# Kernel optimization log

Hardware: AMD Instinct MI355X
Metric: run time of the kernel (lower is better)

Reference implementation:

```python
import jax, jax.numpy as jnp
import numpy as np

B, D, C, P, H, I, E, TOPK = 65536, 1024, 256, 32, 128, 32, 16, 2
FUSION = D + P  # 1056

def ln(x, g, b, eps=1e-5):
    m = jnp.mean(x, axis=-1, keepdims=True)
    v = jnp.mean((x - m) ** 2, axis=-1, keepdims=True)
    return (x - m) * jax.lax.rsqrt(v + eps) * g + b

def setup_inputs() -> dict:
    key = jax.random.key(0)
    ks = jax.random.split(key, 8)
    def w(k, shape):
        return jax.random.normal(k, shape, dtype=jnp.float32) * 0.02
    return {
        "x": jax.random.normal(ks[0], (B, D), dtype=jnp.float32),
        "context": jax.random.normal(ks[1], (B, C), dtype=jnp.float32),
        "en_g": jnp.ones((D,), jnp.float32), "en_b": jnp.zeros((D,), jnp.float32),
        "cn_g": jnp.ones((C,), jnp.float32), "cn_b": jnp.zeros((C,), jnp.float32),
        "cp1_w": w(ks[2], (C, P)), "cp1_b": jnp.zeros((P,), jnp.float32),
        "cp2_w": w(ks[3], (P, P)), "cp2_b": jnp.zeros((P,), jnp.float32),
        "cpn_g": jnp.ones((P,), jnp.float32), "cpn_b": jnp.zeros((P,), jnp.float32),
        "fn_g": jnp.ones((FUSION,), jnp.float32), "fn_b": jnp.zeros((FUSION,), jnp.float32),
        "gp1_w": w(ks[4], (FUSION, H)), "gp1_b": jnp.zeros((H,), jnp.float32),
        "ln1_g": jnp.ones((H,), jnp.float32), "ln1_b": jnp.zeros((H,), jnp.float32),
        "gp2_w": w(ks[5], (H, I)), "gp2_b": jnp.zeros((I,), jnp.float32),
        "ln2_g": jnp.ones((I,), jnp.float32), "ln2_b": jnp.zeros((I,), jnp.float32),
        "gp3_w": w(ks[6], (I, E)), "gp3_b": jnp.zeros((E,), jnp.float32),
    }

def reference(x, context, en_g, en_b, cn_g, cn_b, cp1_w, cp1_b, cp2_w, cp2_b,
              cpn_g, cpn_b, fn_g, fn_b, gp1_w, gp1_b, ln1_g, ln1_b,
              gp2_w, gp2_b, ln2_g, ln2_b, gp3_w, gp3_b):
    gelu = lambda t: jax.nn.gelu(t, approximate=False)  # torch default GELU (erf)
    emb = ln(x, en_g, en_b)                               # [B, D]
    ctx = ln(context, cn_g, cn_b)                         # [B, C]
    cf = gelu(ctx @ cp1_w + cp1_b) @ cp2_w + cp2_b        # [B, P]
    cf = ln(cf, cpn_g, cpn_b)
    fusion = ln(jnp.concatenate([emb, cf], axis=-1), fn_g, fn_b)  # [B, FUSION]
    h = gelu(ln(fusion @ gp1_w + gp1_b, ln1_g, ln1_b))    # [B, H]
    inter = gelu(ln(h @ gp2_w + gp2_b, ln2_g, ln2_b))     # [B, I]
    clean_logits = inter @ gp3_w + gp3_b                  # [B, E]
    # inference path: no noise injection (training=False)
    top_v, top_i = jax.lax.top_k(clean_logits, TOPK)
    combined_weights = jax.nn.softmax(top_v / 1.0, axis=-1)  # temperature=1.0
    return combined_weights, top_i, clean_logits
```

## Files before the change

kernel.cpp:

```cpp
#include <hip/hip_runtime.h>
#include <math.h>

namespace {

using s8v = __attribute__((ext_vector_type(8))) short;
using vf4 = __attribute__((ext_vector_type(4))) float;

constexpr int Bn = 65536;
constexpr int Rn = 64;

constexpr size_t OFF_A1H  = 0;
constexpr size_t OFF_A1M  = 270336;
constexpr size_t OFF_A1L  = 540672;
constexpr size_t OFF_C1H  = 811008;
constexpr size_t OFF_C1M  = 827392;
constexpr size_t OFF_C1L  = 843776;
constexpr size_t OFF_C2H  = 860160;
constexpr size_t OFF_C2M  = 862208;
constexpr size_t OFF_C2L  = 864256;
constexpr size_t OFF_G2H  = 866304;
constexpr size_t OFF_G2M  = 874496;
constexpr size_t OFF_G2L  = 882688;
constexpr size_t OFF_VPK  = 890880;
constexpr size_t OFF_UPK  = 892928;
constexpr size_t OFF_CST  = 893184;
constexpr size_t OFF_VPART= 893216;

__device__ __forceinline__ unsigned short bf16_rn(float f) {
    unsigned u = __float_as_uint(f);
    u += 0x7FFFu + ((u >> 16) & 1u);
    return (unsigned short)(u >> 16);
}
__device__ __forceinline__ float bf16_tof(unsigned short h) {
    return __uint_as_float(((unsigned)h) << 16);
}

union S8U { s8v v; unsigned short u[8]; };

__device__ __forceinline__ vf4 MFMA(s8v a, s8v b, vf4 c) {
    return __builtin_amdgcn_mfma_f32_16x16x32_bf16(a, b, c, 0, 0, 0);
}

__device__ __forceinline__ void mfma6(vf4& acc, s8v ah, s8v am, s8v al,
                                      s8v bh, s8v bm, s8v bl) {
    acc = MFMA(ah, bh, acc);
    acc = MFMA(ah, bm, acc);
    acc = MFMA(am, bh, acc);
    acc = MFMA(ah, bl, acc);
    acc = MFMA(al, bh, acc);
    acc = MFMA(am, bm, acc);
}

__device__ __forceinline__ void split3(float v, unsigned short& h,
                                       unsigned short& m, unsigned short& l) {
    h = bf16_rn(v);
    const float r = v - bf16_tof(h);
    m = bf16_rn(r);
    const float r2 = r - bf16_tof(m);
    l = bf16_rn(r2);
}

__device__ __forceinline__ float gelu_f(float v) {
    return 0.5f * v * (1.0f + erff(v * 0.70710678118654752440f));
}

__device__ __forceinline__ void red16(float& s) {
    s += __shfl_xor(s, 1, 64); s += __shfl_xor(s, 2, 64);
    s += __shfl_xor(s, 4, 64); s += __shfl_xor(s, 8, 64);
}

__global__ void cag_prek1(const float* __restrict__ gp1_w,
                          const float* __restrict__ en_g, const float* __restrict__ en_b,
                          const float* __restrict__ fn_g, const float* __restrict__ fn_b,
                          char* __restrict__ ws)
{
    const int t = threadIdx.x, ch = blockIdx.x;
    s8v* A1h = (s8v*)(ws + OFF_A1H);
    s8v* A1m = (s8v*)(ws + OFF_A1M);
    s8v* A1l = (s8v*)(ws + OFF_A1L);
    float* Vpart = (float*)(ws + OFF_VPART);

    for (int s = t; s < 512; s += 256) {
        const int nt = s >> 6, lane = s & 63;
        const int n = nt * 16 + (lane & 15);
        const int jb = ch * 32 + 8 * (lane >> 4);
        S8U h, m, lo;
        #pragma unroll
        for (int r = 0; r < 8; ++r) {
            const int j = jb + r;
            const float sc = fn_g[j] * (j < 1024 ? en_g[j] : 1.0f);
            const float a = sc * gp1_w[(size_t)j * 128 + n];
            split3(a, h.u[r], m.u[r], lo.u[r]);
        }
        A1h[(ch * 8 + nt) * 64 + lane] = h.v;
        A1m[(ch * 8 + nt) * 64 + lane] = m.v;
        A1l[(ch * 8 + nt) * 64 + lane] = lo.v;
    }
    if (t < 128) {
        float v1 = 0.f, v2 = 0.f, v3 = 0.f, v4 = 0.f;
        for (int jj = 0; jj < 32; ++jj) {
            const int j = ch * 32 + jj;
            const float wv = gp1_w[(size_t)j * 128 + t];
            const float fg = fn_g[j];
            if (j < 1024) { v1 = fmaf(fg * en_g[j], wv, v1); v2 = fmaf(fg * en_b[j], wv, v2); }
            v3 = fmaf(fg, wv, v3);
            v4 = fmaf(fn_b[j], wv, v4);
        }
        float* p = Vpart + ((size_t)ch * 128 + t) * 4;
        p[0] = v1; p[1] = v2; p[2] = v3; p[3] = v4;
    }
}

__global__ void cag_prek2(const float* __restrict__ en_g, const float* __restrict__ en_b,
                          const float* __restrict__ cn_g, const float* __restrict__ cn_b,
                          const float* __restrict__ cp1_w, const float* __restrict__ cp1_b,
                          const float* __restrict__ cp2_w, const float* __restrict__ gp2_w,
                          const float* __restrict__ gp1_b,
                          char* __restrict__ ws)
{
    const int t = threadIdx.x, b = blockIdx.x;
    if (b == 0) {
        const float* Vpart = (const float*)(ws + OFF_VPART);
        float* Vpk = (float*)(ws + OFF_VPK);
        float* cst = (float*)(ws + OFF_CST);
        if (t < 128) {
            float v1 = 0.f, v2 = 0.f, v3 = 0.f, v4 = 0.f;
            for (int ch = 0; ch < 33; ++ch) {
                const float* p = Vpart + ((size_t)ch * 128 + t) * 4;
                v1 += p[0]; v2 += p[1]; v3 += p[2]; v4 += p[3];
            }
            v4 += gp1_b[t];
            float* q = Vpk + t * 4;
            q[0] = v1; q[1] = v2; q[2] = v3; q[3] = v4;
        }
        __shared__ float red[256];
        float part[5] = {0.f, 0.f, 0.f, 0.f, 0.f};
        for (int i = t; i < 1024; i += 256) {
            const float g = en_g[i], bb = en_b[i];
            part[0] += g; part[1] += bb; part[2] += g * g; part[3] += g * bb; part[4] += bb * bb;
        }
        for (int f = 0; f < 5; ++f) {
            red[t] = part[f]; __syncthreads();
            for (int s = 128; s > 0; s >>= 1) { if (t < s) red[t] += red[t + s]; __syncthreads(); }
            if (t == 0) cst[f] = red[0];
            __syncthreads();
        }
    } else if (b == 1) {
        s8v* C1h = (s8v*)(ws + OFF_C1H);
        s8v* C1m = (s8v*)(ws + OFF_C1M);
        s8v* C1l = (s8v*)(ws + OFF_C1L);
        float* up = (float*)(ws + OFF_UPK);
        for (int s = t; s < 8 * 2 * 64; s += 256) {
            const int ks = s >> 7, nt = (s >> 6) & 1, lane = s & 63;
            const int n = nt * 16 + (lane & 15);
            const int kb = ks * 32 + 8 * (lane >> 4);
            S8U h, m, lo;
            #pragma unroll
            for (int r = 0; r < 8; ++r) {
                const int k = kb + r;
                const float a = cn_g[k] * cp1_w[k * 32 + n];
                split3(a, h.u[r], m.u[r], lo.u[r]);
            }
            C1h[(ks * 2 + nt) * 64 + lane] = h.v;
            C1m[(ks * 2 + nt) * 64 + lane] = m.v;
            C1l[(ks * 2 + nt) * 64 + lane] = lo.v;
        }
        if (t < 32) {
            float u1 = 0.f, u2 = 0.f;
            for (int c = 0; c < 256; ++c) {
                u1 = fmaf(cn_g[c], cp1_w[c * 32 + t], u1);
                u2 = fmaf(cn_b[c], cp1_w[c * 32 + t], u2);
            }
            up[2 * t] = u1; up[2 * t + 1] = u2 + cp1_b[t];
        }
    } else if (b == 2) {
        s8v* C2h = (s8v*)(ws + OFF_C2H);
        s8v* C2m = (s8v*)(ws + OFF_C2M);
        s8v* C2l = (s8v*)(ws + OFF_C2L);
        if (t < 128) {
            const int nt = t >> 6, lane = t & 63;
            const int n = nt * 16 + (lane & 15);
            const int kb = 8 * (lane >> 4);
            S8U h, m, lo;
            #pragma unroll
            for (int r = 0; r < 8; ++r) {
                const float a = cp2_w[(kb + r) * 32 + n];
                split3(a, h.u[r], m.u[r], lo.u[r]);
            }
            C2h[nt * 64 + lane] = h.v;
            C2m[nt * 64 + lane] = m.v;
            C2l[nt * 64 + lane] = lo.v;
        }
    } else {
        s8v* G2h = (s8v*)(ws + OFF_G2H);
        s8v* G2m = (s8v*)(ws + OFF_G2M);
        s8v* G2l = (s8v*)(ws + OFF_G2L);
        for (int s = t; s < 4 * 2 * 64; s += 256) {
            const int ks = s >> 7, nt = (s >> 6) & 1, lane = s & 63;
            const int n = nt * 16 + (lane & 15);
            const int kb = ks * 32 + 8 * (lane >> 4);
            S8U h, m, lo;
            #pragma unroll
            for (int r = 0; r < 8; ++r) {
                const float a = gp2_w[(kb + r) * 32 + n];
                split3(a, h.u[r], m.u[r], lo.u[r]);
            }
            G2h[(ks * 2 + nt) * 64 + lane] = h.v;
            G2m[(ks * 2 + nt) * 64 + lane] = m.v;
            G2l[(ks * 2 + nt) * 64 + lane] = lo.v;
        }
    }
}

__global__ __launch_bounds__(256, 2)
void cag_main(const float* __restrict__ x, const float* __restrict__ ctx,
              const float* __restrict__ en_g, const float* __restrict__ en_b,
              const float* __restrict__ cpn_g, const float* __restrict__ cpn_b,
              const float* __restrict__ cp2_b,
              const float* __restrict__ ln1_g, const float* __restrict__ ln1_b,
              const float* __restrict__ gp2_b,
              const float* __restrict__ ln2_g, const float* __restrict__ ln2_b,
              const float* __restrict__ gp3_w, const float* __restrict__ gp3_b,
              const char* __restrict__ ws, float* __restrict__ out)
{
    __shared__ __attribute__((aligned(16))) char smU[64 * 132 * 4];
    __shared__ float cfnbuf[64][36];
    __shared__ float s_sc4[64][4];
    __shared__ float part_s[4][64];
    __shared__ float part_s2[4][64];
    __shared__ float s_ln1[64][2];
    __shared__ float s_cfs[64], s_cfs2[64];

    short (*fragA)[3][4][64][8] = (short(*)[3][4][64][8])smU;
    float (*pbuf)[36]  = (float(*)[36])smU;
    float (*hbuf)[132] = (float(*)[132])smU;
    float (*ibuf)[36]  = (float(*)[36])smU;
    float (*lbuf)[20]  = (float(*)[20])(smU + 16384);

    const int tid = threadIdx.x;
    const int l = tid & 63, w = tid >> 6;
    const int sg = l >> 4, lr = l & 15;
    const int row0 = blockIdx.x * Rn;

    const s8v* A1h = (const s8v*)(ws + OFF_A1H);
    const s8v* A1m = (const s8v*)(ws + OFF_A1M);
    const s8v* A1l = (const s8v*)(ws + OFF_A1L);
    const s8v* C1h = (const s8v*)(ws + OFF_C1H);
    const s8v* C1m = (const s8v*)(ws + OFF_C1M);
    const s8v* C1l = (const s8v*)(ws + OFF_C1L);
    const s8v* C2h = (const s8v*)(ws + OFF_C2H);
    const s8v* C2m = (const s8v*)(ws + OFF_C2M);
    const s8v* C2l = (const s8v*)(ws + OFF_C2L);
    const s8v* G2h = (const s8v*)(ws + OFF_G2H);
    const s8v* G2m = (const s8v*)(ws + OFF_G2M);
    const s8v* G2l = (const s8v*)(ws + OFF_G2L);
    const float* Vpk = (const float*)(ws + OFF_VPK);
    const float* upk = (const float*)(ws + OFF_UPK);
    const float* cst = (const float*)(ws + OFF_CST);

    {
        const int crow = row0 + 16 * w + lr;
        const float* cb = ctx + (size_t)crow * 256 + 8 * sg;
        float cs = 0.f, cs2 = 0.f;
        vf4 ac0 = {0.f, 0.f, 0.f, 0.f}, ac1 = {0.f, 0.f, 0.f, 0.f};
        #pragma unroll
        for (int ks = 0; ks < 8; ++ks) {
            const float4 a0 = *(const float4*)(cb + ks * 32);
            const float4 a1 = *(const float4*)(cb + ks * 32 + 4);
            const float vv[8] = {a0.x, a0.y, a0.z, a0.w, a1.x, a1.y, a1.z, a1.w};
            S8U ah, am, al;
            #pragma unroll
            for (int j = 0; j < 8; ++j) {
                const float v = vv[j];
                cs += v; cs2 = fmaf(v, v, cs2);
                split3(v, ah.u[j], am.u[j], al.u[j]);
            }
            mfma6(ac0, ah.v, am.v, al.v,
                  C1h[(ks * 2 + 0) * 64 + l], C1m[(ks * 2 + 0) * 64 + l], C1l[(ks * 2 + 0) * 64 + l]);
            mfma6(ac1, ah.v, am.v, al.v,
                  C1h[(ks * 2 + 1) * 64 + l], C1m[(ks * 2 + 1) * 64 + l], C1l[(ks * 2 + 1) * 64 + l]);
        }
        cs += __shfl_xor(cs, 16, 64); cs += __shfl_xor(cs, 32, 64);
        cs2 += __shfl_xor(cs2, 16, 64); cs2 += __shfl_xor(cs2, 32, 64);
        const float cm = cs * (1.f / 256.f);
        const float crr = rsqrtf(cs2 * (1.f / 256.f) - cm * cm + 1e-5f);
        float m_r[4], r_r[4];
        #pragma unroll
        for (int rg = 0; rg < 4; ++rg) {
            const int src = 4 * sg + rg;
            m_r[rg] = __shfl(cm, src, 64);
            r_r[rg] = __shfl(crr, src, 64);
        }
        #pragma unroll
        for (int ntl = 0; ntl < 2; ++ntl) {
            const int c = 16 * ntl + lr;
            const float u1 = upk[2 * c], u2 = upk[2 * c + 1];
            #pragma unroll
            for (int rg = 0; rg < 4; ++rg) {
                const float av = (ntl == 0) ? ac0[rg] : ac1[rg];
                const float a1v = r_r[rg] * av - r_r[rg] * m_r[rg] * u1 + u2;
                pbuf[16 * w + 4 * sg + rg][c] = gelu_f(a1v);
            }
        }
        __syncthreads();
        float pv[8];
        const int prow = 16 * w + lr;
        *(float4*)&pv[0] = *(const float4*)&pbuf[prow][8 * sg];
        *(float4*)&pv[4] = *(const float4*)&pbuf[prow][8 * sg + 4];
        S8U ph, pm_, pl;
        #pragma unroll
        for (int j = 0; j < 8; ++j) split3(pv[j], ph.u[j], pm_.u[j], pl.u[j]);
        vf4 a20 = {0.f, 0.f, 0.f, 0.f}, a21 = {0.f, 0.f, 0.f, 0.f};
        mfma6(a20, ph.v, pm_.v, pl.v, C2h[0 * 64 + l], C2m[0 * 64 + l], C2l[0 * 64 + l]);
        mfma6(a21, ph.v, pm_.v, pl.v, C2h[1 * 64 + l], C2m[1 * 64 + l], C2l[1 * 64 + l]);
        const float cb0 = cp2_b[lr], cb1 = cp2_b[16 + lr];
        const float cg0 = cpn_g[lr], cg1 = cpn_g[16 + lr];
        const float cbb0 = cpn_b[lr], cbb1 = cpn_b[16 + lr];
        #pragma unroll
        for (int rg = 0; rg < 4; ++rg) {
            const float v0 = a20[rg] + cb0, v1 = a21[rg] + cb1;
            float s = v0 + v1, s2 = v0 * v0 + v1 * v1;
            red16(s); red16(s2);
            const float pm = s * (1.f / 32.f);
            const float prs = rsqrtf(s2 * (1.f / 32.f) - pm * pm + 1e-5f);
            const float cn0 = (v0 - pm) * prs * cg0 + cbb0;
            const float cn1 = (v1 - pm) * prs * cg1 + cbb1;
            float t = cn0 + cn1, t2 = cn0 * cn0 + cn1 * cn1;
            red16(t); red16(t2);
            const int rr = 16 * w + 4 * sg + rg;
            if (lr == 0) { s_cfs[rr] = t; s_cfs2[rr] = t2; }
            cfnbuf[rr][lr] = cn0; cfnbuf[rr][16 + lr] = cn1;
        }
    }
    __syncthreads();

    float Sx = 0.f, Sxx = 0.f, Sxg = 0.f, Sxg2 = 0.f, Sxgb = 0.f, Sxxg2 = 0.f;
    vf4 acc[4][2];
    #pragma unroll
    for (int mt = 0; mt < 4; ++mt) { acc[mt][0] = vf4{0.f,0.f,0.f,0.f}; acc[mt][1] = vf4{0.f,0.f,0.f,0.f}; }

    const float* xb = x + (size_t)(row0 + 16 * w + lr) * 1024 + 8 * sg;
    float xrinv = 0.f;

    auto stage_x = [&](int c, const float4& a0, const float4& a1) {
        const float vv[8] = {a0.x, a0.y, a0.z, a0.w, a1.x, a1.y, a1.z, a1.w};
        const float4 g0 = *(const float4*)(en_g + c * 32 + 8 * sg);
        const float4 g1 = *(const float4*)(en_g + c * 32 + 8 * sg + 4);
        const float4 e0 = *(const float4*)(en_b + c * 32 + 8 * sg);
        const float4 e1 = *(const float4*)(en_b + c * 32 + 8 * sg + 4);
        const float gg[8] = {g0.x, g0.y, g0.z, g0.w, g1.x, g1.y, g1.z, g1.w};
        const float eb[8] = {e0.x, e0.y, e0.z, e0.w, e1.x, e1.y, e1.z, e1.w};
        S8U hh, mm, ll;
        #pragma unroll
        for (int j = 0; j < 8; ++j) {
            const float v = vv[j], g = gg[j], b = eb[j];
            Sx += v; Sxx = fmaf(v, v, Sxx);
            const float tt = v * g;
            Sxg += tt; Sxg2 = fmaf(tt, g, Sxg2); Sxgb = fmaf(tt, b, Sxgb); Sxxg2 = fmaf(tt, tt, Sxxg2);
            split3(v, hh.u[j], mm.u[j], ll.u[j]);
        }
        *(s8v*)&fragA[c & 1][0][w][l][0] = hh.v;
        *(s8v*)&fragA[c & 1][1][w][l][0] = mm.v;
        *(s8v*)&fragA[c & 1][2][w][l][0] = ll.v;
    };

    {
        const float4 t0 = *(const float4*)(xb + 0), t1 = *(const float4*)(xb + 4);
        float4 xA0 = *(const float4*)(xb + 32), xA1 = *(const float4*)(xb + 36);
        stage_x(0, t0, t1);
        __syncthreads();

        const int nt0 = 2 * w, nt1 = 2 * w + 1;
        s8v bn0h = A1h[(0 * 8 + nt0) * 64 + l], bn0m = A1m[(0 * 8 + nt0) * 64 + l], bn0l = A1l[(0 * 8 + nt0) * 64 + l];
        s8v bn1h = A1h[(0 * 8 + nt1) * 64 + l], bn1m = A1m[(0 * 8 + nt1) * 64 + l], bn1l = A1l[(0 * 8 + nt1) * 64 + l];
        float4 xB0, xB1;

        #pragma unroll 1
        for (int ks = 0; ks <= 32; ++ks) {
            const s8v b0h = bn0h, b0m = bn0m, b0l = bn0l;
            const s8v b1h = bn1h, b1m = bn1m, b1l = bn1l;
            if (ks < 32) {
                bn0h = A1h[((ks + 1) * 8 + nt0) * 64 + l]; bn0m = A1m[((ks + 1) * 8 + nt0) * 64 + l]; bn0l = A1l[((ks + 1) * 8 + nt0) * 64 + l];
                bn1h = A1h[((ks + 1) * 8 + nt1) * 64 + l]; bn1m = A1m[((ks + 1) * 8 + nt1) * 64 + l]; bn1l = A1l[((ks + 1) * 8 + nt1) * 64 + l];
            }
            if (ks + 2 <= 31) {
                xB0 = *(const float4*)(xb + (ks + 2) * 32);
                xB1 = *(const float4*)(xb + (ks + 2) * 32 + 4);
            }
            #pragma unroll
            for (int mt = 0; mt < 4; ++mt) {
                const s8v ah = *(const s8v*)&fragA[ks & 1][0][mt][l][0];
                const s8v am = *(const s8v*)&fragA[ks & 1][1][mt][l][0];
                const s8v al = *(const s8v*)&fragA[ks & 1][2][mt][l][0];
                mfma6(acc[mt][0], ah, am, al, b0h, b0m, b0l);
                mfma6(acc[mt][1], ah, am, al, b1h, b1m, b1l);
            }
            if (ks == 31) {
                float sx = Sx, sxx = Sxx, sxg = Sxg, sxg2 = Sxg2, sxgb = Sxgb, sxxg2 = Sxxg2;
                sx += __shfl_xor(sx, 16, 64); sx += __shfl_xor(sx, 32, 64);
                sxx += __shfl_xor(sxx, 16, 64); sxx += __shfl_xor(sxx, 32, 64);
                sxg += __shfl_xor(sxg, 16, 64); sxg += __shfl_xor(sxg, 32, 64);
                sxg2 += __shfl_xor(sxg2, 16, 64); sxg2 += __shfl_xor(sxg2, 32, 64);
                sxgb += __shfl_xor(sxgb, 16, 64); sxgb += __shfl_xor(sxgb, 32, 64);
                sxxg2 += __shfl_xor(sxxg2, 16, 64); sxxg2 += __shfl_xor(sxxg2, 32, 64);
                const float xm = sx * (1.f / 1024.f);
                const float xvar = sxx * (1.f / 1024.f) - xm * xm;
                const float xr = rsqrtf(xvar + 1e-5f);
                xrinv = sqrtf(xvar + 1e-5f);
                const float Gs = cst[0], Bs = cst[1], Sg2c = cst[2], Sgbc = cst[3], Sb2c = cst[4];
                const float Semb = xr * (sxg - xm * Gs) + Bs;
                const float Semb2 = xr * xr * (sxxg2 - 2.f * xm * sxg2 + xm * xm * Sg2c)
                                  + 2.f * xr * (sxgb - xm * Sgbc) + Sb2c;
                const int rr = 16 * w + lr;
                const float fm = (Semb + s_cfs[rr]) * (1.f / 1056.f);
                const float fvar = (Semb2 + s_cfs2[rr]) * (1.f / 1056.f) - fm * fm;
                const float fr = rsqrtf(fvar + 1e-5f);
                if (sg == 0) {
                    s_sc4[rr][0] = fr * xr;
                    s_sc4[rr][1] = -fr * xr * xm;
                    s_sc4[rr][2] = fr;
                    s_sc4[rr][3] = -fr * fm;
                }
            }
            if (ks < 31) {
                stage_x(ks + 1, xA0, xA1);
                xA0 = xB0; xA1 = xB1;
            } else if (ks == 31) {
                const int rr = 16 * w + lr;
                float vv[8];
                *(float4*)&vv[0] = *(const float4*)&cfnbuf[rr][8 * sg];
                *(float4*)&vv[4] = *(const float4*)&cfnbuf[rr][8 * sg + 4];
                S8U hh, mm, ll;
                #pragma unroll
                for (int j = 0; j < 8; ++j) split3(vv[j] * xrinv, hh.u[j], mm.u[j], ll.u[j]);
                *(s8v*)&fragA[0][0][w][l][0] = hh.v;
                *(s8v*)&fragA[0][1][w][l][0] = mm.v;
                *(s8v*)&fragA[0][2][w][l][0] = ll.v;
            }
            __syncthreads();
        }
    }

    {
        float4 Vc[2];
        #pragma unroll
        for (int ntl = 0; ntl < 2; ++ntl)
            Vc[ntl] = *(const float4*)&Vpk[(16 * (2 * w + ntl) + lr) * 4];
        #pragma unroll
        for (int mt = 0; mt < 4; ++mt) {
            #pragma unroll
            for (int rg = 0; rg < 4; ++rg) {
                const float4 sc = *(const float4*)&s_sc4[16 * mt + 4 * sg + rg][0];
                #pragma unroll
                for (int ntl = 0; ntl < 2; ++ntl) {
                    acc[mt][ntl][rg] = sc.x * acc[mt][ntl][rg] + sc.y * Vc[ntl].x
                                     + sc.z * Vc[ntl].y + sc.w * Vc[ntl].z + Vc[ntl].w;
                }
            }
        }
        #pragma unroll
        for (int mt = 0; mt < 4; ++mt) {
            #pragma unroll
            for (int rg = 0; rg < 4; ++rg) {
                const float v0 = acc[mt][0][rg], v1 = acc[mt][1][rg];
                float s = v0 + v1, s2 = v0 * v0 + v1 * v1;
                red16(s); red16(s2);
                if (lr == 0) {
                    const int rr = 16 * mt + 4 * sg + rg;
                    part_s[w][rr] = s; part_s2[w][rr] = s2;
                }
            }
        }
        __syncthreads();
        if (tid < 64) {
            const float s = part_s[0][tid] + part_s[1][tid] + part_s[2][tid] + part_s[3][tid];
            const float s2 = part_s2[0][tid] + part_s2[1][tid] + part_s2[2][tid] + part_s2[3][tid];
            const float mn = s * (1.f / 128.f);
            s_ln1[tid][0] = mn;
            s_ln1[tid][1] = rsqrtf(s2 * (1.f / 128.f) - mn * mn + 1e-5f);
        }
        __syncthreads();
        float g1c[2], b1c[2];
        #pragma unroll
        for (int ntl = 0; ntl < 2; ++ntl) {
            const int c = 16 * (2 * w + ntl) + lr;
            g1c[ntl] = ln1_g[c]; b1c[ntl] = ln1_b[c];
        }
        #pragma unroll
        for (int mt = 0; mt < 4; ++mt) {
            #pragma unroll
            for (int rg = 0; rg < 4; ++rg) {
                const int rr = 16 * mt + 4 * sg + rg;
                const float mn = s_ln1[rr][0], rs = s_ln1[rr][1];
                #pragma unroll
                for (int ntl = 0; ntl < 2; ++ntl) {
                    const float hp = gelu_f((acc[mt][ntl][rg] - mn) * rs * g1c[ntl] + b1c[ntl]);
                    hbuf[rr][16 * (2 * w + ntl) + lr] = hp;
                }
            }
        }
        __syncthreads();
    }

    float iv[2][4];
    {
        vf4 aG0 = {0.f, 0.f, 0.f, 0.f}, aG1 = {0.f, 0.f, 0.f, 0.f};
        const int hrow = 16 * w + lr;
        #pragma unroll
        for (int ks = 0; ks < 4; ++ks) {
            float pv[8];
            *(float4*)&pv[0] = *(const float4*)&hbuf[hrow][ks * 32 + 8 * sg];
            *(float4*)&pv[4] = *(const float4*)&hbuf[hrow][ks * 32 + 8 * sg + 4];
            S8U ah, am, al;
            #pragma unroll
            for (int j = 0; j < 8; ++j) split3(pv[j], ah.u[j], am.u[j], al.u[j]);
            mfma6(aG0, ah.v, am.v, al.v,
                  G2h[(ks * 2 + 0) * 64 + l], G2m[(ks * 2 + 0) * 64 + l], G2l[(ks * 2 + 0) * 64 + l]);
            mfma6(aG1, ah.v, am.v, al.v,
                  G2h[(ks * 2 + 1) * 64 + l], G2m[(ks * 2 + 1) * 64 + l], G2l[(ks * 2 + 1) * 64 + l]);
        }
        const float gb0 = gp2_b[lr], gb1 = gp2_b[16 + lr];
        const float lg0 = ln2_g[lr], lg1 = ln2_g[16 + lr];
        const float lb0 = ln2_b[lr], lb1 = ln2_b[16 + lr];
        #pragma unroll
        for (int rg = 0; rg < 4; ++rg) {
            const float v0 = aG0[rg] + gb0, v1 = aG1[rg] + gb1;
            float s = v0 + v1, s2 = v0 * v0 + v1 * v1;
            red16(s); red16(s2);
            const float mn = s * (1.f / 32.f);
            const float rs = rsqrtf(s2 * (1.f / 32.f) - mn * mn + 1e-5f);
            iv[0][rg] = gelu_f((v0 - mn) * rs * lg0 + lb0);
            iv[1][rg] = gelu_f((v1 - mn) * rs * lg1 + lb1);
        }
    }
    __syncthreads();
    #pragma unroll
    for (int rg = 0; rg < 4; ++rg) {
        const int rr = 16 * w + 4 * sg + rg;
        ibuf[rr][lr] = iv[0][rg];
        ibuf[rr][16 + lr] = iv[1][rg];
    }
    __syncthreads();

    {
        const int r = tid >> 2, e4 = (tid & 3) * 4;
        float a0 = 0.f, a1 = 0.f, a2 = 0.f, a3 = 0.f;
        #pragma unroll 4
        for (int q = 0; q < 32; ++q) {
            const float v = ibuf[r][q];
            const float4 w3 = *(const float4*)(gp3_w + q * 16 + e4);
            a0 = fmaf(v, w3.x, a0); a1 = fmaf(v, w3.y, a1);
            a2 = fmaf(v, w3.z, a2); a3 = fmaf(v, w3.w, a3);
        }
        const float4 b3 = *(const float4*)(gp3_b + e4);
        const float4 lg = make_float4(a0 + b3.x, a1 + b3.y, a2 + b3.z, a3 + b3.w);
        float* outl = out + (size_t)Bn * 4;
        *(float4*)(outl + (size_t)(row0 + r) * 16 + e4) = lg;
        *(float4*)&lbuf[r][e4] = lg;
    }
    __syncthreads();
    if (tid < 64) {
        float v[16];
        #pragma unroll
        for (int e = 0; e < 4; ++e) *(float4*)&v[e * 4] = *(const float4*)&lbuf[tid][e * 4];
        int i0 = 0; float v0 = v[0];
        #pragma unroll
        for (int e = 1; e < 16; ++e) if (v[e] > v0) { v0 = v[e]; i0 = e; }
        int i1 = -1; float v1 = -3.4e38f;
        #pragma unroll
        for (int e = 0; e < 16; ++e) if (e != i0 && v[e] > v1) { v1 = v[e]; i1 = e; }
        const float e1 = expf(v1 - v0);
        const float inv = 1.0f / (1.0f + e1);
        const size_t g = (size_t)(row0 + tid);
        out[g * 2 + 0] = inv;
        out[g * 2 + 1] = e1 * inv;
        float* outi = out + (size_t)Bn * 2;
        outi[g * 2 + 0] = (float)i0;
        outi[g * 2 + 1] = (float)i1;
    }
}

}

extern "C" void kernel_launch(void* const* d_in, const int* in_sizes, int n_in,
                              void* d_out, int out_size, void* d_ws, size_t ws_size,
                              hipStream_t stream) {
    const float* x     = (const float*)d_in[0];
    const float* ctx   = (const float*)d_in[1];
    const float* en_g  = (const float*)d_in[2];
    const float* en_b  = (const float*)d_in[3];
    const float* cn_g  = (const float*)d_in[4];
    const float* cn_b  = (const float*)d_in[5];
    const float* cp1_w = (const float*)d_in[6];
    const float* cp1_b = (const float*)d_in[7];
    const float* cp2_w = (const float*)d_in[8];
    const float* cp2_b = (const float*)d_in[9];
    const float* cpn_g = (const float*)d_in[10];
    const float* cpn_b = (const float*)d_in[11];
    const float* fn_g  = (const float*)d_in[12];
    const float* fn_b  = (const float*)d_in[13];
    const float* gp1_w = (const float*)d_in[14];
    const float* gp1_b = (const float*)d_in[15];
    const float* ln1_g = (const float*)d_in[16];
    const float* ln1_b = (const float*)d_in[17];
    const float* gp2_w = (const float*)d_in[18];
    const float* gp2_b = (const float*)d_in[19];
    const float* ln2_g = (const float*)d_in[20];
    const float* ln2_b = (const float*)d_in[21];
    const float* gp3_w = (const float*)d_in[22];
    const float* gp3_b = (const float*)d_in[23];

    char* ws = (char*)d_ws;
    hipLaunchKernelGGL(cag_prek1, dim3(33), dim3(256), 0, stream,
                       gp1_w, en_g, en_b, fn_g, fn_b, ws);
    hipLaunchKernelGGL(cag_prek2, dim3(4), dim3(256), 0, stream,
                       en_g, en_b, cn_g, cn_b, cp1_w, cp1_b, cp2_w, gp2_w, gp1_b, ws);
    hipLaunchKernelGGL(cag_main, dim3(Bn / Rn), dim3(256), 0, stream,
                       x, ctx, en_g, en_b, cpn_g, cpn_b, cp2_b,
                       ln1_g, ln1_b, gp2_b, ln2_g, ln2_b, gp3_w, gp3_b,
                       ws, (float*)d_out);
}
```

Before: 212.2 us.

## Use 2x2 warp tiling for first GEMM with register-resident A fragments

Restructures the fusion GEMM so each warp computes a 32-row by 64-column tile: it loads and splits its own x rows directly into registers instead of staging them through shared memory. This removes the per-k-step __syncthreads and LDS round-trip for A, and halves the cross-warp LayerNorm partial reductions. In exchange each warp splits twice as many x values into bf16 pieces, repeating that work across column-warps, and holds more B fragments and accumulators in registers, raising register pressure at two blocks per CU.

Measured after the change: 230.3 us. 1.09x slower.

```diff
diff --git a/kernel.cpp b/kernel.cpp
--- a/kernel.cpp
+++ b/kernel.cpp
@@ -67,6 +67,24 @@
 __device__ __forceinline__ void red16(float& s) {
     s += __shfl_xor(s, 1, 64); s += __shfl_xor(s, 2, 64);
     s += __shfl_xor(s, 4, 64); s += __shfl_xor(s, 8, 64);
+}
+
+__device__ __forceinline__ void stageA(const float4& va, const float4& vb,
+    const float* gg, const float* ee,
+    float& Sx, float& Sxx, float& Sxg, float& Sxg2, float& Sxgb, float& Sq,
+    s8v& fh, s8v& fm, s8v& fl)
+{
+    const float vv[8] = {va.x, va.y, va.z, va.w, vb.x, vb.y, vb.z, vb.w};
+    S8U H, M, L;
+    #pragma unroll
+    for (int j = 0; j < 8; ++j) {
+        const float v = vv[j], g = gg[j], b = ee[j];
+        Sx += v; Sxx = fmaf(v, v, Sxx);
+        const float t = v * g;
+        Sxg += t; Sxg2 = fmaf(t, g, Sxg2); Sxgb = fmaf(t, b, Sxgb); Sq = fmaf(t, t, Sq);
+        split3(v, H.u[j], M.u[j], L.u[j]);
+    }
+    fh = H.v; fm = M.v; fl = L.v;
 }
 
 __global__ void cag_prek1(const float* __restrict__ gp1_w,
@@ -224,18 +242,16 @@
               const char* __restrict__ ws, float* __restrict__ out)
 {
     __shared__ __attribute__((aligned(16))) char smU[64 * 132 * 4];
-    __shared__ float cfnbuf[64][36];
     __shared__ float s_sc4[64][4];
-    __shared__ float part_s[4][64];
-    __shared__ float part_s2[4][64];
-    __shared__ float s_ln1[64][2];
+    __shared__ float part_s[2][64];
+    __shared__ float part_s2[2][64];
     __shared__ float s_cfs[64], s_cfs2[64];
 
-    short (*fragA)[3][4][64][8] = (short(*)[3][4][64][8])smU;
-    float (*pbuf)[36]  = (float(*)[36])smU;
-    float (*hbuf)[132] = (float(*)[132])smU;
-    float (*ibuf)[36]  = (float(*)[36])smU;
-    float (*lbuf)[20]  = (float(*)[20])(smU + 16384);
+    float (*pbuf)[36]   = (float(*)[36])smU;
+    float (*cfnbuf)[36] = (float(*)[36])(smU + 20480);
+    float (*hbuf)[132]  = (float(*)[132])smU;
+    float (*ibuf)[36]   = (float(*)[36])smU;
+    float (*lbuf)[20]   = (float(*)[20])(smU + 16384);
 
     const int tid = threadIdx.x;
     const int l = tid & 63, w = tid >> 6;
@@ -334,168 +350,190 @@
     }
     __syncthreads();
 
-    float Sx = 0.f, Sxx = 0.f, Sxg = 0.f, Sxg2 = 0.f, Sxgb = 0.f, Sxxg2 = 0.f;
-    vf4 acc[4][2];
+    const int a_ = w & 1, c_ = w >> 1;
+    const float* xb0 = x + (size_t)(row0 + 32 * a_ + lr) * 1024 + 8 * sg;
+    const float* xb1 = xb0 + 16 * 1024;
+
+    vf4 acc[2][4];
     #pragma unroll
-    for (int mt = 0; mt < 4; ++mt) { acc[mt][0] = vf4{0.f,0.f,0.f,0.f}; acc[mt][1] = vf4{0.f,0.f,0.f,0.f}; }
-
-    const float* xb = x + (size_t)(row0 + 16 * w + lr) * 1024 + 8 * sg;
-    float xrinv = 0.f;
-
-    auto stage_x = [&](int c, const float4& a0, const float4& a1) {
-        const float vv[8] = {a0.x, a0.y, a0.z, a0.w, a1.x, a1.y, a1.z, a1.w};
-        const float4 g0 = *(const float4*)(en_g + c * 32 + 8 * sg);
-        const float4 g1 = *(const float4*)(en_g + c * 32 + 8 * sg + 4);
-        const float4 e0 = *(const float4*)(en_b + c * 32 + 8 * sg);
-        const float4 e1 = *(const float4*)(en_b + c * 32 + 8 * sg + 4);
+    for (int mt = 0; mt < 2; ++mt)
+        #pragma unroll
+        for (int j = 0; j < 4; ++j) acc[mt][j] = vf4{0.f, 0.f, 0.f, 0.f};
+
+    float s0x = 0.f, s0xx = 0.f, s0xg = 0.f, s0xg2 = 0.f, s0xgb = 0.f, s0q = 0.f;
+    float s1x = 0.f, s1xx = 0.f, s1xg = 0.f, s1xg2 = 0.f, s1xgb = 0.f, s1q = 0.f;
+
+    s8v B0h, B0m, B0l, B1h, B1m, B1l, B2h, B2m, B2l, B3h, B3m, B3l;
+    {
+        const size_t q0 = (size_t)((4 * c_) * 64 + l);
+        B0h = A1h[q0]; B0m = A1m[q0]; B0l = A1l[q0];
+        B1h = A1h[q0 + 64]; B1m = A1m[q0 + 64]; B1l = A1l[q0 + 64];
+    }
+    float4 c0a = *(const float4*)(xb0);
+    float4 c0b = *(const float4*)(xb0 + 4);
+    float4 c1a = *(const float4*)(xb1);
+    float4 c1b = *(const float4*)(xb1 + 4);
+
+    s8v a0h, a0m, a0l, a1h, a1m, a1l;
+
+    #pragma unroll 1
+    for (int ks = 0; ks < 32; ++ks) {
+        const size_t o2 = (size_t)((ks * 8 + 4 * c_ + 2) * 64 + l);
+        B2h = A1h[o2]; B2m = A1m[o2]; B2l = A1l[o2];
+        B3h = A1h[o2 + 64]; B3m = A1m[o2 + 64]; B3l = A1l[o2 + 64];
+        const int kb = ks * 32 + 8 * sg;
+        const float4 g0 = *(const float4*)(en_g + kb);
+        const float4 g1 = *(const float4*)(en_g + kb + 4);
+        const float4 e0 = *(const float4*)(en_b + kb);
+        const float4 e1 = *(const float4*)(en_b + kb + 4);
+        float4 n0a, n0b, n1a, n1b;
+        if (ks < 31) {
+            n0a = *(const float4*)(xb0 + (ks + 1) * 32);
+            n0b = *(const float4*)(xb0 + (ks + 1) * 32 + 4);
+            n1a = *(const float4*)(xb1 + (ks + 1) * 32);
+            n1b = *(const float4*)(xb1 + (ks + 1) * 32 + 4);
+        }
         const float gg[8] = {g0.x, g0.y, g0.z, g0.w, g1.x, g1.y, g1.z, g1.w};
-        const float eb[8] = {e0.x, e0.y, e0.z, e0.w, e1.x, e1.y, e1.z, e1.w};
-        S8U hh, mm, ll;
-        #pragma unroll
-        for (int j = 0; j < 8; ++j) {
-            const float v = vv[j], g = gg[j], b = eb[j];
-            Sx += v; Sxx = fmaf(v, v, Sxx);
-            const float tt = v * g;
-            Sxg += tt; Sxg2 = fmaf(tt, g, Sxg2); Sxgb = fmaf(tt, b, Sxgb); Sxxg2 = fmaf(tt, tt, Sxxg2);
-            split3(v, hh.u[j], mm.u[j], ll.u[j]);
-        }
-        *(s8v*)&fragA[c & 1][0][w][l][0] = hh.v;
-        *(s8v*)&fragA[c & 1][1][w][l][0] = mm.v;
-        *(s8v*)&fragA[c & 1][2][w][l][0] = ll.v;
-    };
-
-    {
-        const float4 t0 = *(const float4*)(xb + 0), t1 = *(const float4*)(xb + 4);
-        float4 xA0 = *(const float4*)(xb + 32), xA1 = *(const float4*)(xb + 36);
-        stage_x(0, t0, t1);
-        __syncthreads();
-
-        const int nt0 = 2 * w, nt1 = 2 * w + 1;
-        s8v bn0h = A1h[(0 * 8 + nt0) * 64 + l], bn0m = A1m[(0 * 8 + nt0) * 64 + l], bn0l = A1l[(0 * 8 + nt0) * 64 + l];
-        s8v bn1h = A1h[(0 * 8 + nt1) * 64 + l], bn1m = A1m[(0 * 8 + nt1) * 64 + l], bn1l = A1l[(0 * 8 + nt1) * 64 + l];
-        float4 xB0, xB1;
-
-        #pragma unroll 1
-        for (int ks = 0; ks <= 32; ++ks) {
-            const s8v b0h = bn0h, b0m = bn0m, b0l = bn0l;
-            const s8v b1h = bn1h, b1m = bn1m, b1l = bn1l;
-            if (ks < 32) {
-                bn0h = A1h[((ks + 1) * 8 + nt0) * 64 + l]; bn0m = A1m[((ks + 1) * 8 + nt0) * 64 + l]; bn0l = A1l[((ks + 1) * 8 + nt0) * 64 + l];
-                bn1h = A1h[((ks + 1) * 8 + nt1) * 64 + l]; bn1m = A1m[((ks + 1) * 8 + nt1) * 64 + l]; bn1l = A1l[((ks + 1) * 8 + nt1) * 64 + l];
-            }
-            if (ks + 2 <= 31) {
-                xB0 = *(const float4*)(xb + (ks + 2) * 32);
-                xB1 = *(const float4*)(xb + (ks + 2) * 32 + 4);
-            }
-            #pragma unroll
-            for (int mt = 0; mt < 4; ++mt) {
-                const s8v ah = *(const s8v*)&fragA[ks & 1][0][mt][l][0];
-                const s8v am = *(const s8v*)&fragA[ks & 1][1][mt][l][0];
-                const s8v al = *(const s8v*)&fragA[ks & 1][2][mt][l][0];
-                mfma6(acc[mt][0], ah, am, al, b0h, b0m, b0l);
-                mfma6(acc[mt][1], ah, am, al, b1h, b1m, b1l);
-            }
-            if (ks == 31) {
-                float sx = Sx, sxx = Sxx, sxg = Sxg, sxg2 = Sxg2, sxgb = Sxgb, sxxg2 = Sxxg2;
-                sx += __shfl_xor(sx, 16, 64); sx += __shfl_xor(sx, 32, 64);
-                sxx += __shfl_xor(sxx, 16, 64); sxx += __shfl_xor(sxx, 32, 64);
-                sxg += __shfl_xor(sxg, 16, 64); sxg += __shfl_xor(sxg, 32, 64);
-                sxg2 += __shfl_xor(sxg2, 16, 64); sxg2 += __shfl_xor(sxg2, 32, 64);
-                sxgb += __shfl_xor(sxgb, 16, 64); sxgb += __shfl_xor(sxgb, 32, 64);
-                sxxg2 += __shfl_xor(sxxg2, 16, 64); sxxg2 += __shfl_xor(sxxg2, 32, 64);
-                const float xm = sx * (1.f / 1024.f);
-                const float xvar = sxx * (1.f / 1024.f) - xm * xm;
-                const float xr = rsqrtf(xvar + 1e-5f);
-                xrinv = sqrtf(xvar + 1e-5f);
-                const float Gs = cst[0], Bs = cst[1], Sg2c = cst[2], Sgbc = cst[3], Sb2c = cst[4];
-                const float Semb = xr * (sxg - xm * Gs) + Bs;
-                const float Semb2 = xr * xr * (sxxg2 - 2.f * xm * sxg2 + xm * xm * Sg2c)
-                                  + 2.f * xr * (sxgb - xm * Sgbc) + Sb2c;
-                const int rr = 16 * w + lr;
-                const float fm = (Semb + s_cfs[rr]) * (1.f / 1056.f);
-                const float fvar = (Semb2 + s_cfs2[rr]) * (1.f / 1056.f) - fm * fm;
-                const float fr = rsqrtf(fvar + 1e-5f);
-                if (sg == 0) {
-                    s_sc4[rr][0] = fr * xr;
-                    s_sc4[rr][1] = -fr * xr * xm;
-                    s_sc4[rr][2] = fr;
-                    s_sc4[rr][3] = -fr * fm;
+        const float ee[8] = {e0.x, e0.y, e0.z, e0.w, e1.x, e1.y, e1.z, e1.w};
+        stageA(c0a, c0b, gg, ee, s0x, s0xx, s0xg, s0xg2, s0xgb, s0q, a0h, a0m, a0l);
+        stageA(c1a, c1b, gg, ee, s1x, s1xx, s1xg, s1xg2, s1xgb, s1q, a1h, a1m, a1l);
+        mfma6(acc[0][0], a0h, a0m, a0l, B0h, B0m, B0l);
+        mfma6(acc[1][0], a1h, a1m, a1l, B0h, B0m, B0l);
+        mfma6(acc[0][1], a0h, a0m, a0l, B1h, B1m, B1l);
+        mfma6(acc[1][1], a1h, a1m, a1l, B1h, B1m, B1l);
+        const size_t p0 = (size_t)(((ks + 1) * 8 + 4 * c_) * 64 + l);
+        B0h = A1h[p0]; B0m = A1m[p0]; B0l = A1l[p0];
+        B1h = A1h[p0 + 64]; B1m = A1m[p0 + 64]; B1l = A1l[p0 + 64];
+        mfma6(acc[0][2], a0h, a0m, a0l, B2h, B2m, B2l);
+        mfma6(acc[1][2], a1h, a1m, a1l, B2h, B2m, B2l);
+        mfma6(acc[0][3], a0h, a0m, a0l, B3h, B3m, B3l);
+        mfma6(acc[1][3], a1h, a1m, a1l, B3h, B3m, B3l);
+        if (ks < 31) { c0a = n0a; c0b = n0b; c1a = n1a; c1b = n1b; }
+    }
+
+    {
+        #define RED2(s) { s += __shfl_xor(s, 16, 64); s += __shfl_xor(s, 32, 64); }
+        RED2(s0x) RED2(s0xx) RED2(s0xg) RED2(s0xg2) RED2(s0xgb) RED2(s0q)
+        RED2(s1x) RED2(s1xx) RED2(s1xg) RED2(s1xg2) RED2(s1xgb) RED2(s1q)
+        #undef RED2
+    }
+    const float Gs = cst[0], Bs = cst[1], Sg2c = cst[2], Sgbc = cst[3], Sb2c = cst[4];
+    float xrinv0, xrinv1;
+    {
+        const float xm = s0x * (1.f / 1024.f);
+        const float xv = s0xx * (1.f / 1024.f) - xm * xm;
+        const float xr = rsqrtf(xv + 1e-5f);
+        xrinv0 = sqrtf(xv + 1e-5f);
+        const float Semb = xr * (s0xg - xm * Gs) + Bs;
+        const float Semb2 = xr * xr * (s0q - 2.f * xm * s0xg2 + xm * xm * Sg2c)
+                          + 2.f * xr * (s0xgb - xm * Sgbc) + Sb2c;
+        const int rr = 32 * a_ + lr;
+        const float fm = (Semb + s_cfs[rr]) * (1.f / 1056.f);
+        const float fvar = (Semb2 + s_cfs2[rr]) * (1.f / 1056.f) - fm * fm;
+        const float fr = rsqrtf(fvar + 1e-5f);
+        if (sg == 0) {
+            s_sc4[rr][0] = fr * xr; s_sc4[rr][1] = -fr * xr * xm;
+            s_sc4[rr][2] = fr;      s_sc4[rr][3] = -fr * fm;
+        }
+    }
+    {
+        const float xm = s1x * (1.f / 1024.f);
+        const float xv = s1xx * (1.f / 1024.f) - xm * xm;
+        const float xr = rsqrtf(xv + 1e-5f);
+        xrinv1 = sqrtf(xv + 1e-5f);
+        const float Semb = xr * (s1xg - xm * Gs) + Bs;
+        const float Semb2 = xr * xr * (s1q - 2.f * xm * s1xg2 + xm * xm * Sg2c)
+                          + 2.f * xr * (s1xgb - xm * Sgbc) + Sb2c;
+        const int rr = 32 * a_ + 16 + lr;
+        const float fm = (Semb + s_cfs[rr]) * (1.f / 1056.f);
+        const float fvar = (Semb2 + s_cfs2[rr]) * (1.f / 1056.f) - fm * fm;
+        const float fr = rsqrtf(fvar + 1e-5f);
+        if (sg == 0) {
+            s_sc4[rr][0] = fr * xr; s_sc4[rr][1] = -fr * xr * xm;
+            s_sc4[rr][2] = fr;      s_sc4[rr][3] = -fr * fm;
+        }
+    }
+    {
+        const int rr0 = 32 * a_ + lr;
+        float vv[8];
+        *(float4*)&vv[0] = *(const float4*)&cfnbuf[rr0][8 * sg];
+        *(float4*)&vv[4] = *(const float4*)&cfnbuf[rr0][8 * sg + 4];
+        S8U H, M, L;
+        #pragma unroll
+        for (int j = 0; j < 8; ++j) split3(vv[j] * xrinv0, H.u[j], M.u[j], L.u[j]);
+        a0h = H.v; a0m = M.v; a0l = L.v;
+        *(float4*)&vv[0] = *(const float4*)&cfnbuf[rr0 + 16][8 * sg];
+        *(float4*)&vv[4] = *(const float4*)&cfnbuf[rr0 + 16][8 * sg + 4];
+        #pragma unroll
+        for (int j = 0; j < 8; ++j) split3(vv[j] * xrinv1, H.u[j], M.u[j], L.u[j]);
+        a1h = H.v; a1m = M.v; a1l = L.v;
+    }
+    {
+        const size_t o2 = (size_t)((32 * 8 + 4 * c_ + 2) * 64 + l);
+        B2h = A1h[o2]; B2m = A1m[o2]; B2l = A1l[o2];
+        B3h = A1h[o2 + 64]; B3m = A1m[o2 + 64]; B3l = A1l[o2 + 64];
+        mfma6(acc[0][0], a0h, a0m, a0l, B0h, B0m, B0l);
+        mfma6(acc[1][0], a1h, a1m, a1l, B0h, B0m, B0l);
+        mfma6(acc[0][1], a0h, a0m, a0l, B1h, B1m, B1l);
+        mfma6(acc[1][1], a1h, a1m, a1l, B1h, B1m, B1l);
+        mfma6(acc[0][2], a0h, a0m, a0l, B2h, B2m, B2l);
+        mfma6(acc[1][2], a1h, a1m, a1l, B2h, B2m, B2l);
+        mfma6(acc[0][3], a0h, a0m, a0l, B3h, B3m, B3l);
+        mfma6(acc[1][3], a1h, a1m, a1l, B3h, B3m, B3l);
+    }
+
+    {
+        float4 Vc[4];
+        #pragma unroll
+        for (int j = 0; j < 4; ++j)
+            Vc[j] = *(const float4*)&Vpk[(64 * c_ + 16 * j + lr) * 4];
+        #pragma unroll
+        for (int mt = 0; mt < 2; ++mt) {
+            #pragma unroll
+            for (int rg = 0; rg < 4; ++rg) {
+                const float4 sc = *(const float4*)&s_sc4[32 * a_ + 16 * mt + 4 * sg + rg][0];
+                #pragma unroll
+                for (int j = 0; j < 4; ++j) {
+                    acc[mt][j][rg] = sc.x * acc[mt][j][rg] + sc.y * Vc[j].x
+                                   + sc.z * Vc[j].y + sc.w * Vc[j].z + Vc[j].w;
                 }
             }
-            if (ks < 31) {
-                stage_x(ks + 1, xA0, xA1);
-                xA0 = xB0; xA1 = xB1;
-            } else if (ks == 31) {
-                const int rr = 16 * w + lr;
-                float vv[8];
-                *(float4*)&vv[0] = *(const float4*)&cfnbuf[rr][8 * sg];
-                *(float4*)&vv[4] = *(const float4*)&cfnbuf[rr][8 * sg + 4];
-                S8U hh, mm, ll;
-                #pragma unroll
-                for (int j = 0; j < 8; ++j) split3(vv[j] * xrinv, hh.u[j], mm.u[j], ll.u[j]);
-                *(s8v*)&fragA[0][0][w][l][0] = hh.v;
-                *(s8v*)&fragA[0][1][w][l][0] = mm.v;
-                *(s8v*)&fragA[0][2][w][l][0] = ll.v;
-            }
-            __syncthreads();
-        }
-    }
-
-    {
-        float4 Vc[2];
-        #pragma unroll
-        for (int ntl = 0; ntl < 2; ++ntl)
-            Vc[ntl] = *(const float4*)&Vpk[(16 * (2 * w + ntl) + lr) * 4];
-        #pragma unroll
-        for (int mt = 0; mt < 4; ++mt) {
-            #pragma unroll
-            for (int rg = 0; rg < 4; ++rg) {
-                const float4 sc = *(const float4*)&s_sc4[16 * mt + 4 * sg + rg][0];
-                #pragma unroll
-                for (int ntl = 0; ntl < 2; ++ntl) {
-                    acc[mt][ntl][rg] = sc.x * acc[mt][ntl][rg] + sc.y * Vc[ntl].x
-                                     + sc.z * Vc[ntl].y + sc.w * Vc[ntl].z + Vc[ntl].w;
-                }
-            }
-        }
-        #pragma unroll
-        for (int mt = 0; mt < 4; ++mt) {
+        }
+        #pragma unroll
+        for (int mt = 0; mt < 2; ++mt) {
             #pragma unroll
             for (int rg = 0; rg < 4; ++rg) {
                 const float v0 = acc[mt][0][rg], v1 = acc[mt][1][rg];
-                float s = v0 + v1, s2 = v0 * v0 + v1 * v1;
+                const float v2 = acc[mt][2][rg], v3 = acc[mt][3][rg];
+                float s = v0 + v1 + v2 + v3;
+                float s2 = v0 * v0 + v1 * v1 + v2 * v2 + v3 * v3;
                 red16(s); red16(s2);
                 if (lr == 0) {
-                    const int rr = 16 * mt + 4 * sg + rg;
-                    part_s[w][rr] = s; part_s2[w][rr] = s2;
+                    const int rr = 32 * a_ + 16 * mt + 4 * sg + rg;
+                    part_s[c_][rr] = s; part_s2[c_][rr] = s2;
                 }
             }
         }
         __syncthreads();
-        if (tid < 64) {
-            const float s = part_s[0][tid] + part_s[1][tid] + part_s[2][tid] + part_s[3][tid];
-            const float s2 = part_s2[0][tid] + part_s2[1][tid] + part_s2[2][tid] + part_s2[3][tid];
-            const float mn = s * (1.f / 128.f);
-            s_ln1[tid][0] = mn;
-            s_ln1[tid][1] = rsqrtf(s2 * (1.f / 128.f) - mn * mn + 1e-5f);
-        }
-        __syncthreads();
-        float g1c[2], b1c[2];
-        #pragma unroll
-        for (int ntl = 0; ntl < 2; ++ntl) {
-            const int c = 16 * (2 * w + ntl) + lr;
-            g1c[ntl] = ln1_g[c]; b1c[ntl] = ln1_b[c];
-        }
-        #pragma unroll
-        for (int mt = 0; mt < 4; ++mt) {
+        float lg1[4], lb1[4];
+        #pragma unroll
+        for (int j = 0; j < 4; ++j) {
+            const int col = 64 * c_ + 16 * j + lr;
+            lg1[j] = ln1_g[col]; lb1[j] = ln1_b[col];
+        }
+        #pragma unroll
+        for (int mt = 0; mt < 2; ++mt) {
             #pragma unroll
             for (int rg = 0; rg < 4; ++rg) {
-                const int rr = 16 * mt + 4 * sg + rg;
-                const float mn = s_ln1[rr][0], rs = s_ln1[rr][1];
+                const int rr = 32 * a_ + 16 * mt + 4 * sg + rg;
+                const float S = part_s[0][rr] + part_s[1][rr];
+                const float S2 = part_s2[0][rr] + part_s2[1][rr];
+                const float mn = S * (1.f / 128.f);
+                const float rs = rsqrtf(S2 * (1.f / 128.f) - mn * mn + 1e-5f);
                 #pragma unroll
-                for (int ntl = 0; ntl < 2; ++ntl) {
-                    const float hp = gelu_f((acc[mt][ntl][rg] - mn) * rs * g1c[ntl] + b1c[ntl]);
-                    hbuf[rr][16 * (2 * w + ntl) + lr] = hp;
+                for (int j = 0; j < 4; ++j) {
+                    const float hp = gelu_f((acc[mt][j][rg] - mn) * rs * lg1[j] + lb1[j]);
+                    hbuf[rr][64 * c_ + 16 * j + lr] = hp;
                 }
             }
         }
```
